# Kernel tuning notes

Hardware: AMD Instinct MI355X
Metric: run time of the kernel (lower is better)

The kernel has to match this reference:

```python
import jax, jax.numpy as jnp
import numpy as np

B, L, HID, H, D = 2, 2048, 1024, 16, 64
ROPE_BASE = 10000.0


def half_rotate(x):
    # [a, b | c, d] -> [-c, -d | a, b] along last dim
    d = x.shape[-1] // 2
    return jnp.concatenate((-x[..., d:], x[..., :d]), axis=-1)


def apply_rope(x, position_ids, base=ROPE_BASE):
    # x: [B, L, H, D]; position_ids: [L] int
    dim = x.shape[-1]
    inv_fre = 1.0 / (base ** (jnp.arange(0, dim, 2, dtype=jnp.float32) / dim))  # [D/2]
    freqs = position_ids.astype(jnp.float32)[None, :, None] * inv_fre  # [1, L, D/2]
    sin = jnp.repeat(jnp.sin(freqs), 2, axis=-1)[:, :, None, :]  # [1, L, 1, D]
    cos = jnp.repeat(jnp.cos(freqs), 2, axis=-1)[:, :, None, :]
    return cos * x + half_rotate(x) * sin


def setup_inputs() -> dict:
    key = jax.random.key(0)
    ks = jax.random.split(key, 5)
    x = jax.random.normal(ks[0], (B, L, HID), dtype=jnp.float32)
    position_id = jnp.arange(L, dtype=jnp.int64)
    # additive causal mask: 0 on/below diagonal, -1e9 above
    causal = jnp.tril(jnp.ones((L, L), dtype=bool))
    atten_mask = jnp.where(causal, 0.0, -1e9).astype(jnp.float32)[None, None]
    s = 1.0 / np.sqrt(HID)
    Wq = jax.random.normal(ks[1], (HID, H * D), dtype=jnp.float32) * s
    Wk = jax.random.normal(ks[2], (HID, H * D), dtype=jnp.float32) * s
    Wv = jax.random.normal(ks[3], (HID, H * D), dtype=jnp.float32) * s
    Wo = jax.random.normal(ks[4], (H * D, HID), dtype=jnp.float32) * s
    return {"x": x, "position_id": position_id, "atten_mask": atten_mask,
            "Wq": Wq, "Wk": Wk, "Wv": Wv, "Wo": Wo}


def reference(x, position_id, atten_mask, Wq, Wk, Wv, Wo):
    b, l, _ = x.shape
    scale = D ** -0.5
    q = (x @ Wq).reshape(b, l, H, D)
    k = (x @ Wk).reshape(b, l, H, D)
    v = (x @ Wv).reshape(b, l, H, D)
    q = apply_rope(q, position_id)
    k = apply_rope(k, position_id)
    # [B, H, Lq, Lk]
    scores = jnp.einsum('bqhd,bkhd->bhqk', q, k) * scale + atten_mask
    attn = jax.nn.softmax(scores.astype(jnp.float32), axis=-1).astype(q.dtype)
    out = jnp.einsum('bhqk,bkhd->bqhd', attn, v).reshape(b, l, H * D)
    return out @ Wo
```

## Files before the change

kernel.cpp:

```cpp
#include <hip/hip_runtime.h>

typedef unsigned short u16;
typedef unsigned int u32;
typedef __attribute__((ext_vector_type(8))) short short8;
typedef __attribute__((ext_vector_type(4))) float f32x4;

#define H_ 16
#define L_ 2048
#define D_ 64
#define HID_ 1024

__device__ __forceinline__ u16 f2bf(float f) {
  union { float f; u32 u; } v; v.f = f;
  u32 r = v.u + 0x7FFFu + ((v.u >> 16) & 1u);
  return (u16)(r >> 16);
}

__device__ __forceinline__ void gl16(const u16* g, u16* l) {
  __builtin_amdgcn_global_load_lds(
      (const __attribute__((address_space(1))) void*)g,
      (__attribute__((address_space(3))) void*)l, 16, 0, 0);
}


__global__ __launch_bounds__(256) void cvt_bf16_k(const float* __restrict__ in,
                                                  u16* __restrict__ out, int n) {
  int i = (blockIdx.x * 256 + threadIdx.x) * 8;
  if (i >= n) return;
  float4 a = *(const float4*)(in + i);
  float4 b = *(const float4*)(in + i + 4);
  u16 r[8] = { f2bf(a.x), f2bf(a.y), f2bf(a.z), f2bf(a.w),
               f2bf(b.x), f2bf(b.y), f2bf(b.z), f2bf(b.w) };
  *(uint4*)(out + i) = *(const uint4*)r;
}

__global__ __launch_bounds__(256) void transpose4_bf_k(
    const float* __restrict__ s0, const float* __restrict__ s1,
    const float* __restrict__ s2, const float* __restrict__ s3,
    u16* __restrict__ d0, u16* __restrict__ d1,
    u16* __restrict__ d2, u16* __restrict__ d3)
{
  __shared__ float t[32][33];
  int w = blockIdx.y;
  const float* in = (w == 0) ? s0 : (w == 1) ? s1 : (w == 2) ? s2 : s3;
  u16* out = (w == 0) ? d0 : (w == 1) ? d1 : (w == 2) ? d2 : d3;
  int bx = blockIdx.x & 31, by = blockIdx.x >> 5;
  int c = threadIdx.x & 31, r0 = threadIdx.x >> 5;
#pragma unroll
  for (int p = 0; p < 4; ++p) {
    int r = r0 + p * 8;
    t[r][c] = in[(size_t)(by * 32 + r) * 1024 + bx * 32 + c];
  }
  __syncthreads();
#pragma unroll
  for (int p = 0; p < 4; ++p) {
    int r = r0 + p * 8;
    out[(size_t)(bx * 32 + r) * 1024 + by * 32 + c] = f2bf(t[c][r]);
  }
}

__global__ __launch_bounds__(256) void rope_tab_k(const int* __restrict__ pos,
                                                  float2* __restrict__ tab) {
  int gid = blockIdx.x * 256 + threadIdx.x;
  int l = gid >> 5, i = gid & 31;
  float p = (float)pos[l];
  float inv = expf(-((float)(2 * i) / 64.0f) * logf(10000.0f));
  float th = p * inv;
  tab[gid] = make_float2(cosf(th), sinf(th));
}


__global__ __launch_bounds__(256) void qkv_gemm_k(
    const u16* __restrict__ A, const u16* __restrict__ Bt,
    u16* __restrict__ Qo, u16* __restrict__ Ko, u16* __restrict__ Vo,
    const float2* __restrict__ rope)
{
  const int K = 1024;
  __shared__ alignas(16) u16 As[2][8192];
  __shared__ alignas(16) u16 Bs[2][12288];
  int tid = threadIdx.x;
  int orig = blockIdx.x;
  int xcd = orig & 7, idx = orig >> 3;
  int px = xcd & 1, py = xcd >> 1;
  int tn = px * 8 + (idx & 7);
  int tm = py * 8 + (idx >> 3);
  int m0 = tm * 128, n0 = tn * 192;
  int prow = tid >> 3;
  int pB = (tid & 7) ^ (prow & 7);
  const u16* gA0 = A + (size_t)(m0 + prow) * K + pB * 8;
  const u16* gB0 = Bt + (size_t)(n0 + prow) * K + pB * 8;
  int wid = tid >> 6, lane = tid & 63, ln = lane & 15, kg = lane >> 4;
  int wm = wid * 32;
  f32x4 acc[2][12] = {};
  int sw0 = (kg ^ (ln & 7)) * 8;
  int sw1 = ((4 + kg) ^ (ln & 7)) * 8;

  auto stage = [&](int kt, int buf) {
#pragma unroll
    for (int s = 0; s < 4; ++s)
      gl16(gA0 + (size_t)s * 32 * K + kt * 64, &As[buf][s * 2048 + tid * 8]);
#pragma unroll
    for (int s = 0; s < 6; ++s)
      gl16(gB0 + (size_t)s * 32 * K + kt * 64, &Bs[buf][s * 2048 + tid * 8]);
  };

  stage(0, 0);
  int cur = 0;
  for (int kt = 0; kt < 16; ++kt) {
    __builtin_amdgcn_s_barrier();
    if (kt + 1 < 16) {
      stage(kt + 1, cur ^ 1);
      asm volatile("s_waitcnt vmcnt(10)" ::: "memory");
    } else {
      asm volatile("s_waitcnt vmcnt(0)" ::: "memory");
    }
    __builtin_amdgcn_sched_barrier(0);
#pragma unroll
    for (int kk = 0; kk < 2; ++kk) {
      int sw = kk ? sw1 : sw0;
      short8 af0 = *(const short8*)&As[cur][(wm + ln) * 64 + sw];
      short8 af1 = *(const short8*)&As[cur][(wm + 16 + ln) * 64 + sw];
#pragma unroll
      for (int nb = 0; nb < 3; ++nb) {
        short8 bq0 = *(const short8*)&Bs[cur][((nb * 64 + 0) + ln) * 64 + sw];
        short8 bq1 = *(const short8*)&Bs[cur][((nb * 64 + 16) + ln) * 64 + sw];
        short8 bq2 = *(const short8*)&Bs[cur][((nb * 64 + 32) + ln) * 64 + sw];
        short8 bq3 = *(const short8*)&Bs[cur][((nb * 64 + 48) + ln) * 64 + sw];
        acc[0][nb * 4 + 0] = __builtin_amdgcn_mfma_f32_16x16x32_bf16(af0, bq0, acc[0][nb * 4 + 0], 0, 0, 0);
        acc[1][nb * 4 + 0] = __builtin_amdgcn_mfma_f32_16x16x32_bf16(af1, bq0, acc[1][nb * 4 + 0], 0, 0, 0);
        acc[0][nb * 4 + 1] = __builtin_amdgcn_mfma_f32_16x16x32_bf16(af0, bq1, acc[0][nb * 4 + 1], 0, 0, 0);
        acc[1][nb * 4 + 1] = __builtin_amdgcn_mfma_f32_16x16x32_bf16(af1, bq1, acc[1][nb * 4 + 1], 0, 0, 0);
        acc[0][nb * 4 + 2] = __builtin_amdgcn_mfma_f32_16x16x32_bf16(af0, bq2, acc[0][nb * 4 + 2], 0, 0, 0);
        acc[1][nb * 4 + 2] = __builtin_amdgcn_mfma_f32_16x16x32_bf16(af1, bq2, acc[1][nb * 4 + 2], 0, 0, 0);
        acc[0][nb * 4 + 3] = __builtin_amdgcn_mfma_f32_16x16x32_bf16(af0, bq3, acc[0][nb * 4 + 3], 0, 0, 0);
        acc[1][nb * 4 + 3] = __builtin_amdgcn_mfma_f32_16x16x32_bf16(af1, bq3, acc[1][nb * 4 + 3], 0, 0, 0);
      }
    }
    cur ^= 1;
  }

#pragma unroll
  for (int hh = 0; hh < 3; ++hh) {
    int gc0 = n0 + hh * 64;
    int sec = gc0 >> 10;
    int h = (gc0 & 1023) >> 6;
    if (sec < 2) {
      u16* Out = (sec == 0) ? Qo : Ko;
      float sc = (sec == 0) ? 0.180336880f : 1.0f;
#pragma unroll
      for (int mi = 0; mi < 2; ++mi)
#pragma unroll
        for (int j = 0; j < 4; ++j) {
          int mm = m0 + wm + mi * 16 + kg * 4 + j;
          int l = mm & (L_ - 1), bb = mm >> 11;
          const float2* tl = rope + l * 32;
#pragma unroll
          for (int g = 0; g < 2; ++g) {
            int dA = g * 16 + ln;
            float xa = acc[mi][hh * 4 + g][j], xb = acc[mi][hh * 4 + g + 2][j];
            float2 fA = tl[dA >> 1];
            float2 fB = tl[16 + (dA >> 1)];
            float oA = (fA.x * xa - fA.y * xb) * sc;
            float oB = (fB.x * xb + fB.y * xa) * sc;
            size_t base = ((size_t)(bb * H_ + h) * L_ + l) * D_;
            Out[base + dA] = f2bf(oA);
            Out[base + dA + 32] = f2bf(oB);
          }
        }
    } else {
#pragma unroll
      for (int mi = 0; mi < 2; ++mi)
#pragma unroll
        for (int j = 0; j < 4; ++j) {
          int mm = m0 + wm + mi * 16 + kg * 4 + j;
          int l = mm & (L_ - 1), bb = mm >> 11;
          size_t base = (size_t)(bb * H_ + h) * (L_ * D_) + (size_t)(l >> 5) * 2048 + (l & 31);
#pragma unroll
          for (int g = 0; g < 4; ++g) {
            int d = g * 16 + ln;
            Vo[base + (size_t)d * 32] = f2bf(acc[mi][hh * 4 + g][j]);
          }
        }
    }
  }
}


__global__ __launch_bounds__(256) void oproj_k(
    const u16* __restrict__ A, const u16* __restrict__ Bt, float* __restrict__ Out)
{
  const int K = 1024;
  __shared__ alignas(16) u16 As[2][2048];
  __shared__ alignas(16) u16 Bs[2][4096];
  int tid = threadIdx.x;
  int orig = blockIdx.x;
  int xcd = orig & 7, idx = orig >> 3;
  int px = xcd & 1, py = xcd >> 1;
  int tn = px * 4 + (idx & 3);
  int tm = py * 16 + (idx >> 2);
  int m0 = tm * 64, n0 = tn * 128;
  int line = tid >> 3, bp = tid & 7;
  int blkS = bp ^ (line & 7);
  int srow = 2 * line + (blkS >> 2);
  int scol = (blkS & 3) * 8;
  const u16* gA = A + (size_t)(m0 + srow) * K + scol;
  const u16* gB = Bt + (size_t)(n0 + srow) * K + scol;
  int wid = tid >> 6, lane = tid & 63, ln = lane & 15, kg = lane >> 4;
  int wm = (wid >> 1) * 32, wn = (wid & 1) * 64;
  f32x4 acc[2][4] = {};
  int lhalf = ln >> 1, lpar = ln & 1;
  int sb = ((lpar << 2) | kg) ^ lhalf;
  int baseA = ((wm >> 1) + lhalf) * 64 + sb * 8;
  int baseB = ((wn >> 1) + lhalf) * 64 + sb * 8;

  auto stage = [&](int buf, int kt) {
    gl16(gA + kt * 32, &As[buf][tid * 8]);
    const u16* gb = gB + kt * 32;
    gl16(gb, &Bs[buf][tid * 8]);
    gl16(gb + 64 * K, &Bs[buf][2048 + tid * 8]);
  };

  stage(0, 0);
  asm volatile("s_waitcnt vmcnt(0)" ::: "memory");
  __syncthreads();
  int cur = 0;
  for (int kt = 0; kt < 32; ++kt) {
    if (kt < 31) stage(cur ^ 1, kt + 1);
    short8 af[2], bfr[4];
#pragma unroll
    for (int i = 0; i < 2; ++i) af[i] = *(const short8*)&As[cur][baseA + i * 512];
#pragma unroll
    for (int i = 0; i < 4; ++i) bfr[i] = *(const short8*)&Bs[cur][baseB + i * 512];
#pragma unroll
    for (int mi = 0; mi < 2; ++mi)
#pragma unroll
      for (int ni = 0; ni < 4; ++ni)
        acc[mi][ni] = __builtin_amdgcn_mfma_f32_16x16x32_bf16(af[mi], bfr[ni], acc[mi][ni], 0, 0, 0);
    __syncthreads();
    cur ^= 1;
  }
#pragma unroll
  for (int mi = 0; mi < 2; ++mi)
#pragma unroll
    for (int j = 0; j < 4; ++j) {
      int mm = m0 + wm + mi * 16 + kg * 4 + j;
#pragma unroll
      for (int ni = 0; ni < 4; ++ni)
        Out[(size_t)mm * 1024 + n0 + wn + ni * 16 + ln] = acc[mi][ni][j];
    }
}

__global__ __launch_bounds__(256) void attn_k(
    const u16* __restrict__ Q, const u16* __restrict__ K,
    const u16* __restrict__ V, u16* __restrict__ AO)
{
  __shared__ alignas(16) u16 Ks[2][8192];
  __shared__ alignas(16) u16 Vs[2][8192];
  int tid = threadIdx.x;
  int wid = tid >> 6, lane = tid & 63;
  int ln = lane & 15, kg = lane >> 4;
  int orig = blockIdx.x;
  int swz = (orig & 7) * 64 + (orig >> 3);
  int bh = swz >> 4;
  int i = swz & 15;
  int tA = i, tB = 31 - i;
  int nA = (tA >> 1) + 1;
  int nB = (tB >> 1) + 1;
  const int NCH = 17;
  int q0A = tA * 64 + wid * 16;
  int q0B = tB * 64 + wid * 16;
  const u16* Qh = Q + (size_t)bh * L_ * D_;
  const u16* Kh = K + (size_t)bh * L_ * D_;
  const u16* Vt = V + (size_t)bh * L_ * D_;

  int srow = tid >> 3, sblk = tid & 7;
  const u16* kb = Kh + (size_t)srow * 64 + ((sblk ^ (srow & 7)) << 3);
  const u16* vb = Vt + (size_t)(tid >> 2) * 32 + (((tid & 3) ^ ((tid >> 3) & 3)) << 3);

  short8 qfA0 = *(const short8*)(Qh + (size_t)(q0A + ln) * D_ + kg * 8);
  short8 qfA1 = *(const short8*)(Qh + (size_t)(q0A + ln) * D_ + 32 + kg * 8);
  short8 qfB0 = *(const short8*)(Qh + (size_t)(q0B + ln) * D_ + kg * 8);
  short8 qfB1 = *(const short8*)(Qh + (size_t)(q0B + ln) * D_ + 32 + kg * 8);

  f32x4 oA[4] = {}, oB[4] = {};
  float lsA = 0.f, lsB = 0.f;
  int srcA = ln + (((2 * kg) & 3) << 4);
  int srcB = ln + (((2 * kg + 1) & 3) << 4);
  bool thi = (kg >= 2);
  int sw0 = (kg ^ (ln & 7)) * 8;
  int sw1 = ((4 + kg) ^ (ln & 7)) * 8;
  int vsw = (kg ^ ((ln >> 1) & 3)) * 8;
  int jdA = (tA & 1) * 4 + wid;
  int jdB = (tB & 1) * 4 + wid;

  auto stage = [&](int chunk, int buf) {
    const u16* kc = kb + (size_t)chunk * 8192;
    const u16* vc = vb + (size_t)chunk * 8192;
#pragma unroll
    for (int s2 = 0; s2 < 4; ++s2) {
      gl16(kc + s2 * 2048, &Ks[buf][s2 * 2048 + tid * 8]);
      gl16(vc + s2 * 2048, &Vs[buf][s2 * 2048 + tid * 8]);
    }
  };
  auto seq = [&](int c) { return (c < nA) ? c : c - nA; };

  auto step = [&](int cur, int jd, short8 qf0, short8 qf1,
                  float& lsum, f32x4 (&o)[4]) {
    f32x4 s[8];
    __builtin_amdgcn_s_setprio(1);
#pragma unroll
    for (int j = 0; j < 8; ++j) {
      short8 ka = *(const short8*)&Ks[cur][(j * 16 + ln) * 64 + sw0];
      short8 kc = *(const short8*)&Ks[cur][(j * 16 + ln) * 64 + sw1];
      f32x4 t = {};
      t = __builtin_amdgcn_mfma_f32_16x16x32_bf16(ka, qf0, t, 0, 0, 0);
      t = __builtin_amdgcn_mfma_f32_16x16x32_bf16(kc, qf1, t, 0, 0, 0);
      s[j] = t;
    }
    __builtin_amdgcn_s_setprio(0);
    if (jd < 8) {
#pragma unroll
      for (int j = 0; j < 8; ++j)
#pragma unroll
        for (int r = 0; r < 4; ++r) {
          bool kill = (j > jd) | ((j == jd) & ((kg * 4 + r) > ln));
          if (kill) s[j][r] = -1e30f;
        }
    }
    float ps = 0.f;
    u32 wA[8], wB[8];
#pragma unroll
    for (int j = 0; j < 8; ++j) {
      float p0, p1, p2, p3;
      asm("v_exp_f32 %0, %1" : "=v"(p0) : "v"(s[j][0]));
      asm("v_exp_f32 %0, %1" : "=v"(p1) : "v"(s[j][1]));
      asm("v_exp_f32 %0, %1" : "=v"(p2) : "v"(s[j][2]));
      asm("v_exp_f32 %0, %1" : "=v"(p3) : "v"(s[j][3]));
      ps += (p0 + p1) + (p2 + p3);
      asm("v_cvt_pk_bf16_f32 %0, %1, %2" : "=v"(wA[j]) : "v"(p0), "v"(p1));
      asm("v_cvt_pk_bf16_f32 %0, %1, %2" : "=v"(wB[j]) : "v"(p2), "v"(p3));
    }
    lsum += ps;
#pragma unroll
    for (int g = 0; g < 4; ++g) {
      int j0 = 2 * g, j1 = j0 + 1;
      u32 a0 = __shfl((int)wA[j0], srcA), a1 = __shfl((int)wA[j1], srcA);
      u32 b0 = __shfl((int)wB[j0], srcA), b1 = __shfl((int)wB[j1], srcA);
      u32 c0 = __shfl((int)wA[j0], srcB), c1 = __shfl((int)wA[j1], srcB);
      u32 e0 = __shfl((int)wB[j0], srcB), e1 = __shfl((int)wB[j1], srcB);
      union { u32 u[4]; short8 s8; } pu;
      pu.u[0] = thi ? a1 : a0;
      pu.u[1] = thi ? b1 : b0;
      pu.u[2] = thi ? c1 : c0;
      pu.u[3] = thi ? e1 : e0;
      short8 vf0 = *(const short8*)&Vs[cur][g * 2048 + ln * 32 + vsw];
      short8 vf1 = *(const short8*)&Vs[cur][g * 2048 + (16 + ln) * 32 + vsw];
      short8 vf2 = *(const short8*)&Vs[cur][g * 2048 + (32 + ln) * 32 + vsw];
      short8 vf3 = *(const short8*)&Vs[cur][g * 2048 + (48 + ln) * 32 + vsw];
      __builtin_amdgcn_s_setprio(1);
      o[0] = __builtin_amdgcn_mfma_f32_16x16x32_bf16(vf0, pu.s8, o[0], 0, 0, 0);
      o[1] = __builtin_amdgcn_mfma_f32_16x16x32_bf16(vf1, pu.s8, o[1], 0, 0, 0);
      o[2] = __builtin_amdgcn_mfma_f32_16x16x32_bf16(vf2, pu.s8, o[2], 0, 0, 0);
      o[3] = __builtin_amdgcn_mfma_f32_16x16x32_bf16(vf3, pu.s8, o[3], 0, 0, 0);
      __builtin_amdgcn_s_setprio(0);
    }
  };

  stage(seq(0), 0);
  int cur = 0;

  for (int c = 0; c < NCH; ++c) {
    __builtin_amdgcn_s_barrier();
    if (c + 1 < NCH) {
      stage(seq(c + 1), cur ^ 1);
      asm volatile("s_waitcnt vmcnt(8)" ::: "memory");
    } else {
      asm volatile("s_waitcnt vmcnt(0)" ::: "memory");
    }
    __builtin_amdgcn_sched_barrier(0);

    if (c < nA) {
      step(cur, (c == nA - 1) ? jdA : 8, qfA0, qfA1, lsA, oA);
    } else {
      int cl = c - nA;
      step(cur, (cl == nB - 1) ? jdB : 8, qfB0, qfB1, lsB, oB);
    }
    cur ^= 1;
  }

  int b = bh >> 4, h = bh & 15;
  lsA += __shfl_xor(lsA, 16);
  lsA += __shfl_xor(lsA, 32);
  lsB += __shfl_xor(lsB, 16);
  lsB += __shfl_xor(lsB, 32);
  float invA = 1.0f / lsA, invB = 1.0f / lsB;
  u16* rowA = AO + ((size_t)(b * L_ + q0A + ln) * H_ + h) * D_;
  u16* rowB = AO + ((size_t)(b * L_ + q0B + ln) * H_ + h) * D_;
#pragma unroll
  for (int dt = 0; dt < 4; ++dt) {
    union { u16 pk[4]; uint2 v; } uA, uB;
#pragma unroll
    for (int r = 0; r < 4; ++r) {
      uA.pk[r] = f2bf(oA[dt][r] * invA);
      uB.pk[r] = f2bf(oB[dt][r] * invB);
    }
    *(uint2*)(rowA + dt * 16 + kg * 4) = uA.v;
    *(uint2*)(rowB + dt * 16 + kg * 4) = uB.v;
  }
}


extern "C" void kernel_launch(void* const* d_in, const int* in_sizes, int n_in,
                              void* d_out, int out_size, void* d_ws, size_t ws_size,
                              hipStream_t stream) {
  (void)in_sizes; (void)n_in; (void)out_size; (void)ws_size;
  const float* x   = (const float*)d_in[0];
  const int*   pos = (const int*)d_in[1];
  const float* Wq  = (const float*)d_in[3];
  const float* Wk  = (const float*)d_in[4];
  const float* Wv  = (const float*)d_in[5];
  const float* Wo  = (const float*)d_in[6];

  char* ws = (char*)d_ws;
  u16* xbf = (u16*)ws;
  u16* Wt3 = (u16*)(ws + (size_t)( 8 << 20));
  u16* Wto = (u16*)(ws + (size_t)(14 << 20));
  u16* Qb  = (u16*)(ws + (size_t)(16 << 20));
  u16* Kb  = (u16*)(ws + (size_t)(24 << 20));
  u16* Vt  = (u16*)(ws + (size_t)(32 << 20));
  u16* AO  = (u16*)(ws + (size_t)(40 << 20));
  float2* tab = (float2*)(ws + (size_t)(48 << 20));

  cvt_bf16_k<<<2048, 256, 0, stream>>>(x, xbf, 4096 * 1024);
  transpose4_bf_k<<<dim3(1024, 4), 256, 0, stream>>>(
      Wq, Wk, Wv, Wo, Wt3, Wt3 + (size_t)1048576, Wt3 + (size_t)2097152, Wto);
  rope_tab_k<<<256, 256, 0, stream>>>(pos, tab);
  qkv_gemm_k<<<512, 256, 0, stream>>>(xbf, Wt3, Qb, Kb, Vt, tab);
  attn_k<<<512, 256, 0, stream>>>(Qb, Kb, Vt, AO);
  oproj_k<<<512, 256, 0, stream>>>(AO, Wto, (float*)d_out);
}
```

Baseline: 114.3 us.

## Split causal tile pair across waves and share K/V chunks between both tiles

Instead of every wave walking tile A then tile B sequentially (17 chunks), waves 0-1 now own tile A and waves 2-3 own tile B, each wave computing 32 query rows. K/V chunks are staged once per chunk index and used by both tile groups, so the loop runs nB chunks instead of nA+nB. This halves K/V staging traffic and reuses each K/V LDS fragment for two query blocks. The tradeoff is load imbalance: tile-A waves sit idle in later iterations while tile-B waves still compute, and per-wave register use doubles.

```diff
diff --git a/kernel.cpp b/kernel.cpp
--- a/kernel.cpp
+++ b/kernel.cpp
@@ -266,9 +266,10 @@
   int tA = i, tB = 31 - i;
   int nA = (tA >> 1) + 1;
   int nB = (tB >> 1) + 1;
-  const int NCH = 17;
-  int q0A = tA * 64 + wid * 16;
-  int q0B = tB * 64 + wid * 16;
+  int myTile = (wid >> 1) ? tB : tA;
+  int myN = (wid >> 1) ? nB : nA;
+  int w2 = wid & 1;
+  int q0 = myTile * 64 + w2 * 32;
   const u16* Qh = Q + (size_t)bh * L_ * D_;
   const u16* Kh = K + (size_t)bh * L_ * D_;
   const u16* Vt = V + (size_t)bh * L_ * D_;
@@ -277,21 +278,20 @@
   const u16* kb = Kh + (size_t)srow * 64 + ((sblk ^ (srow & 7)) << 3);
   const u16* vb = Vt + (size_t)(tid >> 2) * 32 + (((tid & 3) ^ ((tid >> 3) & 3)) << 3);
 
-  short8 qfA0 = *(const short8*)(Qh + (size_t)(q0A + ln) * D_ + kg * 8);
-  short8 qfA1 = *(const short8*)(Qh + (size_t)(q0A + ln) * D_ + 32 + kg * 8);
-  short8 qfB0 = *(const short8*)(Qh + (size_t)(q0B + ln) * D_ + kg * 8);
-  short8 qfB1 = *(const short8*)(Qh + (size_t)(q0B + ln) * D_ + 32 + kg * 8);
-
-  f32x4 oA[4] = {}, oB[4] = {};
-  float lsA = 0.f, lsB = 0.f;
+  short8 qf00 = *(const short8*)(Qh + (size_t)(q0 + ln) * D_ + kg * 8);
+  short8 qf01 = *(const short8*)(Qh + (size_t)(q0 + ln) * D_ + 32 + kg * 8);
+  short8 qf10 = *(const short8*)(Qh + (size_t)(q0 + 16 + ln) * D_ + kg * 8);
+  short8 qf11 = *(const short8*)(Qh + (size_t)(q0 + 16 + ln) * D_ + 32 + kg * 8);
+
+  f32x4 o0[4] = {}, o1[4] = {};
+  float ls0 = 0.f, ls1 = 0.f;
   int srcA = ln + (((2 * kg) & 3) << 4);
   int srcB = ln + (((2 * kg + 1) & 3) << 4);
   bool thi = (kg >= 2);
   int sw0 = (kg ^ (ln & 7)) * 8;
   int sw1 = ((4 + kg) ^ (ln & 7)) * 8;
   int vsw = (kg ^ ((ln >> 1) & 3)) * 8;
-  int jdA = (tA & 1) * 4 + wid;
-  int jdB = (tB & 1) * 4 + wid;
+  int jdbase = (myTile & 1) * 4 + w2 * 2;
 
   auto stage = [&](int chunk, int buf) {
     const u16* kc = kb + (size_t)chunk * 8192;
@@ -302,110 +302,130 @@
       gl16(vc + s2 * 2048, &Vs[buf][s2 * 2048 + tid * 8]);
     }
   };
-  auto seq = [&](int c) { return (c < nA) ? c : c - nA; };
-
-  auto step = [&](int cur, int jd, short8 qf0, short8 qf1,
-                  float& lsum, f32x4 (&o)[4]) {
-    f32x4 s[8];
-    __builtin_amdgcn_s_setprio(1);
-#pragma unroll
-    for (int j = 0; j < 8; ++j) {
-      short8 ka = *(const short8*)&Ks[cur][(j * 16 + ln) * 64 + sw0];
-      short8 kc = *(const short8*)&Ks[cur][(j * 16 + ln) * 64 + sw1];
-      f32x4 t = {};
-      t = __builtin_amdgcn_mfma_f32_16x16x32_bf16(ka, qf0, t, 0, 0, 0);
-      t = __builtin_amdgcn_mfma_f32_16x16x32_bf16(kc, qf1, t, 0, 0, 0);
-      s[j] = t;
-    }
-    __builtin_amdgcn_s_setprio(0);
-    if (jd < 8) {
-#pragma unroll
-      for (int j = 0; j < 8; ++j)
-#pragma unroll
-        for (int r = 0; r < 4; ++r) {
-          bool kill = (j > jd) | ((j == jd) & ((kg * 4 + r) > ln));
-          if (kill) s[j][r] = -1e30f;
-        }
-    }
-    float ps = 0.f;
-    u32 wA[8], wB[8];
-#pragma unroll
-    for (int j = 0; j < 8; ++j) {
-      float p0, p1, p2, p3;
-      asm("v_exp_f32 %0, %1" : "=v"(p0) : "v"(s[j][0]));
-      asm("v_exp_f32 %0, %1" : "=v"(p1) : "v"(s[j][1]));
-      asm("v_exp_f32 %0, %1" : "=v"(p2) : "v"(s[j][2]));
-      asm("v_exp_f32 %0, %1" : "=v"(p3) : "v"(s[j][3]));
-      ps += (p0 + p1) + (p2 + p3);
-      asm("v_cvt_pk_bf16_f32 %0, %1, %2" : "=v"(wA[j]) : "v"(p0), "v"(p1));
-      asm("v_cvt_pk_bf16_f32 %0, %1, %2" : "=v"(wB[j]) : "v"(p2), "v"(p3));
-    }
-    lsum += ps;
-#pragma unroll
-    for (int g = 0; g < 4; ++g) {
-      int j0 = 2 * g, j1 = j0 + 1;
-      u32 a0 = __shfl((int)wA[j0], srcA), a1 = __shfl((int)wA[j1], srcA);
-      u32 b0 = __shfl((int)wB[j0], srcA), b1 = __shfl((int)wB[j1], srcA);
-      u32 c0 = __shfl((int)wA[j0], srcB), c1 = __shfl((int)wA[j1], srcB);
-      u32 e0 = __shfl((int)wB[j0], srcB), e1 = __shfl((int)wB[j1], srcB);
-      union { u32 u[4]; short8 s8; } pu;
-      pu.u[0] = thi ? a1 : a0;
-      pu.u[1] = thi ? b1 : b0;
-      pu.u[2] = thi ? c1 : c0;
-      pu.u[3] = thi ? e1 : e0;
-      short8 vf0 = *(const short8*)&Vs[cur][g * 2048 + ln * 32 + vsw];
-      short8 vf1 = *(const short8*)&Vs[cur][g * 2048 + (16 + ln) * 32 + vsw];
-      short8 vf2 = *(const short8*)&Vs[cur][g * 2048 + (32 + ln) * 32 + vsw];
-      short8 vf3 = *(const short8*)&Vs[cur][g * 2048 + (48 + ln) * 32 + vsw];
-      __builtin_amdgcn_s_setprio(1);
-      o[0] = __builtin_amdgcn_mfma_f32_16x16x32_bf16(vf0, pu.s8, o[0], 0, 0, 0);
-      o[1] = __builtin_amdgcn_mfma_f32_16x16x32_bf16(vf1, pu.s8, o[1], 0, 0, 0);
-      o[2] = __builtin_amdgcn_mfma_f32_16x16x32_bf16(vf2, pu.s8, o[2], 0, 0, 0);
-      o[3] = __builtin_amdgcn_mfma_f32_16x16x32_bf16(vf3, pu.s8, o[3], 0, 0, 0);
-      __builtin_amdgcn_s_setprio(0);
-    }
-  };
-
-  stage(seq(0), 0);
+
+  stage(0, 0);
   int cur = 0;
 
-  for (int c = 0; c < NCH; ++c) {
+  for (int c = 0; c < nB; ++c) {
     __builtin_amdgcn_s_barrier();
-    if (c + 1 < NCH) {
-      stage(seq(c + 1), cur ^ 1);
+    if (c + 1 < nB) {
+      stage(c + 1, cur ^ 1);
       asm volatile("s_waitcnt vmcnt(8)" ::: "memory");
     } else {
       asm volatile("s_waitcnt vmcnt(0)" ::: "memory");
     }
     __builtin_amdgcn_sched_barrier(0);
 
-    if (c < nA) {
-      step(cur, (c == nA - 1) ? jdA : 8, qfA0, qfA1, lsA, oA);
-    } else {
-      int cl = c - nA;
-      step(cur, (cl == nB - 1) ? jdB : 8, qfB0, qfB1, lsB, oB);
+    if (c < myN) {
+      int jd0 = (c == myN - 1) ? jdbase : 8;
+      f32x4 s0[8], s1[8];
+      __builtin_amdgcn_s_setprio(1);
+#pragma unroll
+      for (int j = 0; j < 8; ++j) {
+        short8 ka = *(const short8*)&Ks[cur][(j * 16 + ln) * 64 + sw0];
+        short8 kc = *(const short8*)&Ks[cur][(j * 16 + ln) * 64 + sw1];
+        f32x4 t = {};
+        t = __builtin_amdgcn_mfma_f32_16x16x32_bf16(ka, qf00, t, 0, 0, 0);
+        t = __builtin_amdgcn_mfma_f32_16x16x32_bf16(kc, qf01, t, 0, 0, 0);
+        s0[j] = t;
+        f32x4 u = {};
+        u = __builtin_amdgcn_mfma_f32_16x16x32_bf16(ka, qf10, u, 0, 0, 0);
+        u = __builtin_amdgcn_mfma_f32_16x16x32_bf16(kc, qf11, u, 0, 0, 0);
+        s1[j] = u;
+      }
+      __builtin_amdgcn_s_setprio(0);
+      if (jd0 < 8) {
+        int jd1 = jd0 + 1;
+#pragma unroll
+        for (int j = 0; j < 8; ++j)
+#pragma unroll
+          for (int r = 0; r < 4; ++r) {
+            bool k0 = (j > jd0) | ((j == jd0) & ((kg * 4 + r) > ln));
+            if (k0) s0[j][r] = -1e30f;
+            bool k1 = (j > jd1) | ((j == jd1) & ((kg * 4 + r) > ln));
+            if (k1) s1[j][r] = -1e30f;
+          }
+      }
+      float ps0 = 0.f, ps1 = 0.f;
+      u32 wA0[8], wB0[8], wA1[8], wB1[8];
+#pragma unroll
+      for (int j = 0; j < 8; ++j) {
+        float a0, a1, a2, a3, b0, b1, b2, b3;
+        asm("v_exp_f32 %0, %1" : "=v"(a0) : "v"(s0[j][0]));
+        asm("v_exp_f32 %0, %1" : "=v"(a1) : "v"(s0[j][1]));
+        asm("v_exp_f32 %0, %1" : "=v"(a2) : "v"(s0[j][2]));
+        asm("v_exp_f32 %0, %1" : "=v"(a3) : "v"(s0[j][3]));
+        asm("v_exp_f32 %0, %1" : "=v"(b0) : "v"(s1[j][0]));
+        asm("v_exp_f32 %0, %1" : "=v"(b1) : "v"(s1[j][1]));
+        asm("v_exp_f32 %0, %1" : "=v"(b2) : "v"(s1[j][2]));
+        asm("v_exp_f32 %0, %1" : "=v"(b3) : "v"(s1[j][3]));
+        ps0 += (a0 + a1) + (a2 + a3);
+        ps1 += (b0 + b1) + (b2 + b3);
+        asm("v_cvt_pk_bf16_f32 %0, %1, %2" : "=v"(wA0[j]) : "v"(a0), "v"(a1));
+        asm("v_cvt_pk_bf16_f32 %0, %1, %2" : "=v"(wB0[j]) : "v"(a2), "v"(a3));
+        asm("v_cvt_pk_bf16_f32 %0, %1, %2" : "=v"(wA1[j]) : "v"(b0), "v"(b1));
+        asm("v_cvt_pk_bf16_f32 %0, %1, %2" : "=v"(wB1[j]) : "v"(b2), "v"(b3));
+      }
+      ls0 += ps0;
+      ls1 += ps1;
+#pragma unroll
+      for (int g = 0; g < 4; ++g) {
+        int j0 = 2 * g, j1 = j0 + 1;
+        u32 x0 = __shfl((int)wA0[j0], srcA), x1 = __shfl((int)wA0[j1], srcA);
+        u32 x2 = __shfl((int)wB0[j0], srcA), x3 = __shfl((int)wB0[j1], srcA);
+        u32 x4 = __shfl((int)wA0[j0], srcB), x5 = __shfl((int)wA0[j1], srcB);
+        u32 x6 = __shfl((int)wB0[j0], srcB), x7 = __shfl((int)wB0[j1], srcB);
+        union { u32 u[4]; short8 s8; } pu0;
+        pu0.u[0] = thi ? x1 : x0;
+        pu0.u[1] = thi ? x3 : x2;
+        pu0.u[2] = thi ? x5 : x4;
+        pu0.u[3] = thi ? x7 : x6;
+        u32 y0 = __shfl((int)wA1[j0], srcA), y1 = __shfl((int)wA1[j1], srcA);
+        u32 y2 = __shfl((int)wB1[j0], srcA), y3 = __shfl((int)wB1[j1], srcA);
+        u32 y4 = __shfl((int)wA1[j0], srcB), y5 = __shfl((int)wA1[j1], srcB);
+        u32 y6 = __shfl((int)wB1[j0], srcB), y7 = __shfl((int)wB1[j1], srcB);
+        union { u32 u[4]; short8 s8; } pu1;
+        pu1.u[0] = thi ? y1 : y0;
+        pu1.u[1] = thi ? y3 : y2;
+        pu1.u[2] = thi ? y5 : y4;
+        pu1.u[3] = thi ? y7 : y6;
+        short8 vf0 = *(const short8*)&Vs[cur][g * 2048 + ln * 32 + vsw];
+        short8 vf1 = *(const short8*)&Vs[cur][g * 2048 + (16 + ln) * 32 + vsw];
+        short8 vf2 = *(const short8*)&Vs[cur][g * 2048 + (32 + ln) * 32 + vsw];
+        short8 vf3 = *(const short8*)&Vs[cur][g * 2048 + (48 + ln) * 32 + vsw];
+        __builtin_amdgcn_s_setprio(1);
+        o0[0] = __builtin_amdgcn_mfma_f32_16x16x32_bf16(vf0, pu0.s8, o0[0], 0, 0, 0);
+        o0[1] = __builtin_amdgcn_mfma_f32_16x16x32_bf16(vf1, pu0.s8, o0[1], 0, 0, 0);
+        o0[2] = __builtin_amdgcn_mfma_f32_16x16x32_bf16(vf2, pu0.s8, o0[2], 0, 0, 0);
+        o0[3] = __builtin_amdgcn_mfma_f32_16x16x32_bf16(vf3, pu0.s8, o0[3], 0, 0, 0);
+        o1[0] = __builtin_amdgcn_mfma_f32_16x16x32_bf16(vf0, pu1.s8, o1[0], 0, 0, 0);
+        o1[1] = __builtin_amdgcn_mfma_f32_16x16x32_bf16(vf1, pu1.s8, o1[1], 0, 0, 0);
+        o1[2] = __builtin_amdgcn_mfma_f32_16x16x32_bf16(vf2, pu1.s8, o1[2], 0, 0, 0);
+        o1[3] = __builtin_amdgcn_mfma_f32_16x16x32_bf16(vf3, pu1.s8, o1[3], 0, 0, 0);
+        __builtin_amdgcn_s_setprio(0);
+      }
     }
     cur ^= 1;
   }
 
   int b = bh >> 4, h = bh & 15;
-  lsA += __shfl_xor(lsA, 16);
-  lsA += __shfl_xor(lsA, 32);
-  lsB += __shfl_xor(lsB, 16);
-  lsB += __shfl_xor(lsB, 32);
-  float invA = 1.0f / lsA, invB = 1.0f / lsB;
-  u16* rowA = AO + ((size_t)(b * L_ + q0A + ln) * H_ + h) * D_;
-  u16* rowB = AO + ((size_t)(b * L_ + q0B + ln) * H_ + h) * D_;
+  ls0 += __shfl_xor(ls0, 16);
+  ls0 += __shfl_xor(ls0, 32);
+  ls1 += __shfl_xor(ls1, 16);
+  ls1 += __shfl_xor(ls1, 32);
+  float inv0 = 1.0f / ls0, inv1 = 1.0f / ls1;
+  u16* row0 = AO + ((size_t)(b * L_ + q0 + ln) * H_ + h) * D_;
+  u16* row1 = AO + ((size_t)(b * L_ + q0 + 16 + ln) * H_ + h) * D_;
 #pragma unroll
   for (int dt = 0; dt < 4; ++dt) {
-    union { u16 pk[4]; uint2 v; } uA, uB;
+    union { u16 pk[4]; uint2 v; } u0, u1;
 #pragma unroll
     for (int r = 0; r < 4; ++r) {
-      uA.pk[r] = f2bf(oA[dt][r] * invA);
-      uB.pk[r] = f2bf(oB[dt][r] * invB);
-    }
-    *(uint2*)(rowA + dt * 16 + kg * 4) = uA.v;
-    *(uint2*)(rowB + dt * 16 + kg * 4) = uB.v;
+      u0.pk[r] = f2bf(o0[dt][r] * inv0);
+      u1.pk[r] = f2bf(o1[dt][r] * inv1);
+    }
+    *(uint2*)(row0 + dt * 16 + kg * 4) = u0.v;
+    *(uint2*)(row1 + dt * 16 + kg * 4) = u1.v;
   }
 }
 
```

New measurement: 124.1 us. +8.6%, slower.

## Double oproj K-tile to 64 and restructure prefetch with partial vmcnt waits

Applied to the files above, without the earlier changes.

The output-projection GEMM now stages 64-wide K tiles instead of 32, halving the number of main-loop iterations and barriers, and uses a new XOR swizzle on 64-element LDS rows. The prefetch is issued after a single barrier at the top of each iteration, and a partial vmcnt wait lets the next tile's global-to-LDS loads stay in flight while the current tile is consumed. This doubles LDS use per block and relies on careful ordering of the wait counter for correctness.

```diff
diff --git a/kernel.cpp b/kernel.cpp
--- a/kernel.cpp
+++ b/kernel.cpp
@@ -190,8 +190,8 @@
     const u16* __restrict__ A, const u16* __restrict__ Bt, float* __restrict__ Out)
 {
   const int K = 1024;
-  __shared__ alignas(16) u16 As[2][2048];
-  __shared__ alignas(16) u16 Bs[2][4096];
+  __shared__ alignas(16) u16 As[2][4096];
+  __shared__ alignas(16) u16 Bs[2][8192];
   int tid = threadIdx.x;
   int orig = blockIdx.x;
   int xcd = orig & 7, idx = orig >> 3;
@@ -199,44 +199,50 @@
   int tn = px * 4 + (idx & 3);
   int tm = py * 16 + (idx >> 2);
   int m0 = tm * 64, n0 = tn * 128;
-  int line = tid >> 3, bp = tid & 7;
-  int blkS = bp ^ (line & 7);
-  int srow = 2 * line + (blkS >> 2);
-  int scol = (blkS & 3) * 8;
-  const u16* gA = A + (size_t)(m0 + srow) * K + scol;
-  const u16* gB = Bt + (size_t)(n0 + srow) * K + scol;
+  int prow = tid >> 3;
+  int pB = (tid & 7) ^ (prow & 7);
+  const u16* gA0 = A + (size_t)(m0 + prow) * K + pB * 8;
+  const u16* gB0 = Bt + (size_t)(n0 + prow) * K + pB * 8;
   int wid = tid >> 6, lane = tid & 63, ln = lane & 15, kg = lane >> 4;
   int wm = (wid >> 1) * 32, wn = (wid & 1) * 64;
   f32x4 acc[2][4] = {};
-  int lhalf = ln >> 1, lpar = ln & 1;
-  int sb = ((lpar << 2) | kg) ^ lhalf;
-  int baseA = ((wm >> 1) + lhalf) * 64 + sb * 8;
-  int baseB = ((wn >> 1) + lhalf) * 64 + sb * 8;
-
-  auto stage = [&](int buf, int kt) {
-    gl16(gA + kt * 32, &As[buf][tid * 8]);
-    const u16* gb = gB + kt * 32;
-    gl16(gb, &Bs[buf][tid * 8]);
-    gl16(gb + 64 * K, &Bs[buf][2048 + tid * 8]);
+  int sw0 = (kg ^ (ln & 7)) * 8;
+  int sw1 = ((4 + kg) ^ (ln & 7)) * 8;
+
+  auto stage = [&](int kt, int buf) {
+#pragma unroll
+    for (int s = 0; s < 2; ++s)
+      gl16(gA0 + (size_t)s * 32 * K + kt * 64, &As[buf][s * 2048 + tid * 8]);
+#pragma unroll
+    for (int s = 0; s < 4; ++s)
+      gl16(gB0 + (size_t)s * 32 * K + kt * 64, &Bs[buf][s * 2048 + tid * 8]);
   };
 
   stage(0, 0);
-  asm volatile("s_waitcnt vmcnt(0)" ::: "memory");
-  __syncthreads();
   int cur = 0;
-  for (int kt = 0; kt < 32; ++kt) {
-    if (kt < 31) stage(cur ^ 1, kt + 1);
-    short8 af[2], bfr[4];
-#pragma unroll
-    for (int i = 0; i < 2; ++i) af[i] = *(const short8*)&As[cur][baseA + i * 512];
-#pragma unroll
-    for (int i = 0; i < 4; ++i) bfr[i] = *(const short8*)&Bs[cur][baseB + i * 512];
-#pragma unroll
-    for (int mi = 0; mi < 2; ++mi)
-#pragma unroll
-      for (int ni = 0; ni < 4; ++ni)
-        acc[mi][ni] = __builtin_amdgcn_mfma_f32_16x16x32_bf16(af[mi], bfr[ni], acc[mi][ni], 0, 0, 0);
-    __syncthreads();
+  for (int kt = 0; kt < 16; ++kt) {
+    __builtin_amdgcn_s_barrier();
+    if (kt + 1 < 16) {
+      stage(kt + 1, cur ^ 1);
+      asm volatile("s_waitcnt vmcnt(6)" ::: "memory");
+    } else {
+      asm volatile("s_waitcnt vmcnt(0)" ::: "memory");
+    }
+    __builtin_amdgcn_sched_barrier(0);
+#pragma unroll
+    for (int kk = 0; kk < 2; ++kk) {
+      int sw = kk ? sw1 : sw0;
+      short8 af[2], bfr[4];
+#pragma unroll
+      for (int i = 0; i < 2; ++i) af[i] = *(const short8*)&As[cur][(wm + i * 16 + ln) * 64 + sw];
+#pragma unroll
+      for (int i = 0; i < 4; ++i) bfr[i] = *(const short8*)&Bs[cur][(wn + i * 16 + ln) * 64 + sw];
+#pragma unroll
+      for (int mi = 0; mi < 2; ++mi)
+#pragma unroll
+        for (int ni = 0; ni < 4; ++ni)
+          acc[mi][ni] = __builtin_amdgcn_mfma_f32_16x16x32_bf16(af[mi], bfr[ni], acc[mi][ni], 0, 0, 0);
+    }
     cur ^= 1;
   }
 #pragma unroll
```

After: 106.9 us. 1.07x faster.
